# Kernel optimization log

Measured on AMD Instinct MI355X. Metric: run time of the kernel, lower is better.

## Reference

```python
import jax, jax.numpy as jnp
import numpy as np

B, T, D, S, K = 8, 4096, 1024, 64, 3
EPS = 1e-5

def setup_inputs() -> dict:
    key = jax.random.key(0)
    ks = jax.random.split(key, 10)
    def lin(k, out_d, in_d):
        s = 1.0 / np.sqrt(in_d)
        return jax.random.uniform(k, (out_d, in_d), jnp.float32, -s, s)
    return {
        "x": jax.random.normal(ks[0], (B, T, D), jnp.float32),
        "norm_w": jnp.ones((D,), jnp.float32),
        "norm_b": jnp.zeros((D,), jnp.float32),
        "in_w": lin(ks[1], 2 * D, D),
        "in_b": jnp.zeros((2 * D,), jnp.float32),
        "conv_w": jax.random.normal(ks[2], (D, 1, K), jnp.float32) / np.sqrt(K),
        "conv_b": jnp.zeros((D,), jnp.float32),
        "dt_w": lin(ks[3], S, D),
        "dt_b": jnp.zeros((S,), jnp.float32),
        "b_w": lin(ks[4], S, D),
        "b_b": jnp.zeros((S,), jnp.float32),
        "c_w": lin(ks[5], S, D),
        "c_b": jnp.zeros((S,), jnp.float32),
        "a_log": jax.random.normal(ks[6], (S,), jnp.float32) * 0.02,
        "d": jnp.ones((D,), jnp.float32),
        "out_w": lin(ks[7], D, D + S),
        "out_b": jnp.zeros((D,), jnp.float32),
    }

def reference(x, norm_w, norm_b, in_w, in_b, conv_w, conv_b,
              dt_w, dt_b, b_w, b_b, c_w, c_b, a_log, d, out_w, out_b):
    bsz, tlen, dim = x.shape
    sdim = a_log.shape[0]
    k = conv_w.shape[-1]
    residual = x
    # LayerNorm
    mu = jnp.mean(x, axis=-1, keepdims=True)
    var = jnp.mean(jnp.square(x - mu), axis=-1, keepdims=True)
    xn = (x - mu) * jax.lax.rsqrt(var + EPS) * norm_w + norm_b
    # in_proj and chunk
    h = xn @ in_w.T + in_b                       # (B,T,2D)
    x_proj, z = jnp.split(h, 2, axis=-1)         # each (B,T,D)
    # depthwise conv over time, 'same' padding
    xc = jax.lax.conv_general_dilated(
        x_proj.transpose(0, 2, 1), conv_w, (1,), [(k // 2, k // 2)],
        dimension_numbers=("NCH", "OIH", "NCH"), feature_group_count=dim)
    x_conv = jnp.tanh((xc + conv_b[None, :, None]).transpose(0, 2, 1))  # (B,T,D)
    # gate projections for all timesteps at once
    dt = jax.nn.softplus(z @ dt_w.T + dt_b) + 1e-4   # (B,T,S)
    b = jnp.tanh(z @ b_w.T + b_b)                    # (B,T,S)
    c = jnp.tanh(z @ c_w.T + c_b)                    # (B,T,S)
    a = -jnp.exp(a_log)                              # (S,)
    decay = jnp.exp(a * dt)                          # (B,T,S)
    # linear recurrence: state_t = state_{t-1} * decay_t + b_t
    def step(state, inp):
        dec_t, b_t = inp
        state = state * dec_t + b_t
        return state, state
    _, states = jax.lax.scan(step, jnp.zeros((bsz, sdim), x.dtype),
                             (decay.transpose(1, 0, 2), b.transpose(1, 0, 2)))
    states = states.transpose(1, 0, 2)               # (B,T,S)
    y = c * states
    mix = jnp.concatenate([x_conv * d, y], axis=-1)  # (B,T,D+S)
    out = mix @ out_w.T + out_b                      # (B,T,D)
    return residual + out
```

## Files before the change

kernel.cpp:

```cpp
#include <hip/hip_runtime.h>

#define TT 4096
#define DD 1024
#define NN 32768

typedef short s16x8 __attribute__((ext_vector_type(8)));
typedef float f32x4 __attribute__((ext_vector_type(4)));
typedef unsigned short ushort_t;

__device__ __forceinline__ unsigned short f2bf(float f) {
  unsigned u = __float_as_uint(f);
  u += 0x7FFFu + ((u >> 16) & 1u);
  return (unsigned short)(u >> 16);
}
__device__ __forceinline__ float bf2f(unsigned short h) {
  return __uint_as_float(((unsigned)h) << 16);
}
__device__ __forceinline__ void load_lds16(const void* g, void* l) {
  __builtin_amdgcn_global_load_lds(
      (const __attribute__((address_space(1))) unsigned int*)g,
      (__attribute__((address_space(3))) unsigned int*)l, 16, 0, 0);
}

__global__ __launch_bounds__(256)
void cvt_kernel(const float* __restrict__ s, ushort_t* __restrict__ d, int n) {
  int i = (blockIdx.x * 256 + threadIdx.x) * 4;
  if (i < n) {
    float4 v = *(const float4*)&s[i];
    ushort4 o; o.x = f2bf(v.x); o.y = f2bf(v.y); o.z = f2bf(v.z); o.w = f2bf(v.w);
    *(ushort4*)&d[i] = o;
  }
}

__global__ __launch_bounds__(256)
void w3pad_kernel(const float* __restrict__ dt_w, const float* __restrict__ b_w,
                  const float* __restrict__ c_w, ushort_t* __restrict__ w3) {
  int e = (blockIdx.x * 256 + threadIdx.x) * 4;
  int row = e >> 10, col = e & 1023;
  float4 v; v.x = 0.f; v.y = 0.f; v.z = 0.f; v.w = 0.f;
  if (row < 64)       v = *(const float4*)&dt_w[(row << 10) + col];
  else if (row < 128) v = *(const float4*)&b_w[((row - 64) << 10) + col];
  else if (row < 192) v = *(const float4*)&c_w[((row - 128) << 10) + col];
  ushort4 o; o.x = f2bf(v.x); o.y = f2bf(v.y); o.z = f2bf(v.z); o.w = f2bf(v.w);
  *(ushort4*)&w3[e] = o;
}

__global__ __launch_bounds__(256)
void ln_kernel(const float* __restrict__ x, const float* __restrict__ w,
               const float* __restrict__ bv, ushort_t* __restrict__ xn)
{
  int row = blockIdx.x * 4 + (threadIdx.x >> 6);
  int lane = threadIdx.x & 63;
  const float* xr = x + (size_t)row * DD;
  float4 v[4];
  float s = 0.f, ss = 0.f;
  #pragma unroll
  for (int j = 0; j < 4; ++j) {
    v[j] = *(const float4*)&xr[j * 256 + lane * 4];
    s  += v[j].x + v[j].y + v[j].z + v[j].w;
    ss += v[j].x * v[j].x + v[j].y * v[j].y + v[j].z * v[j].z + v[j].w * v[j].w;
  }
  #pragma unroll
  for (int off = 32; off > 0; off >>= 1) {
    s  += __shfl_xor(s, off, 64);
    ss += __shfl_xor(ss, off, 64);
  }
  float mean = s * (1.f / 1024.f);
  float var  = ss * (1.f / 1024.f) - mean * mean;
  float rinv = rsqrtf(var + 1e-5f);
  #pragma unroll
  for (int j = 0; j < 4; ++j) {
    int c = j * 256 + lane * 4;
    float4 wv = *(const float4*)&w[c];
    float4 bb = *(const float4*)&bv[c];
    ushort4 o;
    o.x = f2bf((v[j].x - mean) * rinv * wv.x + bb.x);
    o.y = f2bf((v[j].y - mean) * rinv * wv.y + bb.y);
    o.z = f2bf((v[j].z - mean) * rinv * wv.z + bb.z);
    o.w = f2bf((v[j].w - mean) * rinv * wv.w + bb.w);
    *(ushort4*)&xn[(size_t)row * DD + c] = o;
  }
}

template<int EP>
__global__ __launch_bounds__(512, 2)
void gemm256(const ushort_t* __restrict__ A, const ushort_t* __restrict__ W,
             int M, int N, int K,
             const float* __restrict__ bias0, const float* __restrict__ bias1,
             const float* __restrict__ bias2, const float* __restrict__ alog,
             ushort_t* __restrict__ o0, ushort_t* __restrict__ o1,
             float* __restrict__ g0, float* __restrict__ g1, float* __restrict__ g2,
             const float* __restrict__ resid, float* __restrict__ outf)
{
  __shared__ ushort_t lds[65536];
  const int tid = threadIdx.x;
  const int lane = tid & 63;
  const int wid = tid >> 6;
  const int wr = wid >> 2;
  const int wc = wid & 3;
  const int lane15 = lane & 15;
  const int lgrp = lane >> 4;
  const int rsw = (lane15 & 7) << 4;
  const int ntn = N >> 8;
  int bid = blockIdx.x;
  { const int cpx = (int)gridDim.x >> 3; bid = (bid & 7) * cpx + (bid >> 3); }
  const int brow = (bid / ntn) << 8;
  const int bcol = (bid % ntn) << 8;
  const int nk = K >> 6;
  const int sRow = tid >> 3;
  const int sCol = (tid & 7) << 4;
  const char* ldsb = (const char*)lds;
  (void)M;

#define STG(bufb, isB, h, kt) do { \
    const int ktc_ = (kt) < nk ? (kt) : nk - 1; \
    const ushort_t* gsrc_ = (isB) ? W : A; \
    const int rowb_ = ((isB) ? bcol : brow) + (h) * 128; \
    _Pragma("unroll") \
    for (int j_ = 0; j_ < 2; ++j_) { \
      const int r_ = j_ * 64 + sRow; \
      load_lds16((const char*)(gsrc_ + (size_t)(rowb_ + r_) * K) + ktc_ * 128 + (sCol ^ ((r_ & 7) << 4)), \
                 (char*)lds + (bufb) * 65536 + (isB) * 32768 + (h) * 16384 + r_ * 128 + sCol); \
    } } while (0)

#define LDA_(bufb, m, kk) \
  (*(const s16x8*)(ldsb + (bufb) * 65536 + wr * 16384 + ((m) * 16 + lane15) * 128 + (((kk) * 64 + lgrp * 16) ^ rsw)))
#define LDB_(bufb, n, kk) \
  (*(const s16x8*)(ldsb + (bufb) * 65536 + 32768 + (wc >> 1) * 16384 + ((wc & 1) * 64 + (n) * 16 + lane15) * 128 + (((kk) * 64 + lgrp * 16) ^ rsw)))

#define BARR() asm volatile("s_barrier" ::: "memory")
#define VMW4() asm volatile("s_waitcnt vmcnt(4)" ::: "memory")
#define SBAR() __builtin_amdgcn_sched_barrier(0)

#define RD_A(bufb, mh) do { \
    _Pragma("unroll") for (int kk = 0; kk < 2; ++kk) \
    _Pragma("unroll") for (int q = 0; q < 4; ++q) \
      af[kk][q] = LDA_(bufb, (mh) * 4 + q, kk); } while (0)
#define RD_B(bufb, nh) do { \
    _Pragma("unroll") for (int kk = 0; kk < 2; ++kk) \
    _Pragma("unroll") for (int p = 0; p < 2; ++p) \
      bfr[nh][kk][p] = LDB_(bufb, (nh) * 2 + p, kk); } while (0)

#define MFMAQ(mh, nh) do { \
    __builtin_amdgcn_s_setprio(1); \
    _Pragma("unroll") for (int kk = 0; kk < 2; ++kk) \
    _Pragma("unroll") for (int q = 0; q < 4; ++q) \
    _Pragma("unroll") for (int p = 0; p < 2; ++p) \
      acc[(mh) * 4 + q][(nh) * 2 + p] = __builtin_amdgcn_mfma_f32_16x16x32_bf16( \
          af[kk][q], bfr[nh][kk][p], acc[(mh) * 4 + q][(nh) * 2 + p], 0, 0, 0); \
    __builtin_amdgcn_s_setprio(0); } while (0)

  f32x4 acc[8][4];
  #pragma unroll
  for (int m = 0; m < 8; ++m) {
    #pragma unroll
    for (int n = 0; n < 4; ++n) acc[m][n] = (f32x4){0.f, 0.f, 0.f, 0.f};
  }
  s16x8 af[2][4];
  s16x8 bfr[2][2][2];

  STG(0, 1, 0, 0); STG(0, 0, 0, 0); STG(0, 0, 1, 0); STG(0, 1, 1, 0);
  STG(1, 1, 0, 1); STG(1, 0, 0, 1);
  VMW4(); BARR();
  RD_A(0, 0); RD_B(0, 0);

  const int nIter = nk >> 1;
  for (int it = 0; it < nIter; ++it) {
    const int t0 = 2 * it;
    STG(1, 0, 1, t0 + 1);
    MFMAQ(0, 0); SBAR(); RD_B(0, 1); BARR();
    STG(1, 1, 1, t0 + 1);
    MFMAQ(0, 1); SBAR(); RD_A(0, 1); BARR();
    STG(0, 1, 0, t0 + 2);
    MFMAQ(1, 1); BARR();
    STG(0, 0, 0, t0 + 2);
    VMW4(); BARR();
    MFMAQ(1, 0); SBAR(); RD_A(1, 0); RD_B(1, 0); BARR();
    STG(0, 0, 1, t0 + 2);
    MFMAQ(0, 0); SBAR(); RD_B(1, 1); BARR();
    STG(0, 1, 1, t0 + 2);
    MFMAQ(0, 1); SBAR(); RD_A(1, 1); BARR();
    STG(1, 1, 0, t0 + 3);
    MFMAQ(1, 1); BARR();
    STG(1, 0, 0, t0 + 3);
    VMW4(); BARR();
    MFMAQ(1, 0); SBAR(); RD_A(0, 0); RD_B(0, 0); BARR();
  }
  if (nk & 1) {
    MFMAQ(0, 0); SBAR(); RD_B(0, 1);
    MFMAQ(0, 1); SBAR(); RD_A(0, 1);
    MFMAQ(1, 1);
    MFMAQ(1, 0);
  }

#undef STG
#undef LDA_
#undef LDB_
#undef BARR
#undef VMW4
#undef SBAR
#undef RD_A
#undef RD_B
#undef MFMAQ

  #pragma unroll
  for (int m = 0; m < 8; ++m) {
    #pragma unroll
    for (int i = 0; i < 4; ++i) {
      const int r = brow + wr * 128 + m * 16 + lgrp * 4 + i;
      #pragma unroll
      for (int n = 0; n < 4; ++n) {
        const int col = bcol + wc * 64 + n * 16 + lane15;
        float v = acc[m][n][i];
        if constexpr (EP == 0) {
          v += bias0[col];
          if (col < DD) o0[(size_t)r * DD + col] = f2bf(v);
          else          o1[(size_t)r * DD + (col - DD)] = f2bf(v);
        } else if constexpr (EP == 1) {
          if (col < 64) {
            float u = v + bias0[col];
            float sp = (u > 20.f) ? u : log1pf(expf(u));
            float dt = sp + 1e-4f;
            float a = -expf(alog[col]);
            g0[(size_t)r * 64 + col] = expf(a * dt);
          } else if (col < 128) {
            g1[(size_t)r * 64 + (col - 64)] = tanhf(v + bias1[col - 64]);
          } else if (col < 192) {
            g2[(size_t)r * 64 + (col - 128)] = tanhf(v + bias2[col - 128]);
          }
        } else {
          outf[(size_t)r * DD + col] = v + bias0[col] + resid[(size_t)r * DD + col];
        }
      }
    }
  }
}

template<int EP>
__global__ __launch_bounds__(256)
void gemm128(const ushort_t* __restrict__ A, const ushort_t* __restrict__ W,
             int M, int N, int K,
             const float* __restrict__ bias0, const float* __restrict__ bias1,
             const float* __restrict__ bias2, const float* __restrict__ alog,
             float* __restrict__ g0, float* __restrict__ g1, float* __restrict__ g2)
{
  __shared__ ushort_t As[128 * 64];
  __shared__ ushort_t Bs[128 * 64];
  const int tid = threadIdx.x;
  const int lane = tid & 63;
  const int wid = tid >> 6;
  const int ntn = N >> 7;
  const int brow = (blockIdx.x / ntn) << 7;
  const int bcol = (blockIdx.x % ntn) << 7;
  const int wr = (wid >> 1) << 6;
  const int wc = (wid & 1) << 6;
  const int lane15 = lane & 15;
  const int lgrp = lane >> 4;

  f32x4 acc[4][4];
  #pragma unroll
  for (int m = 0; m < 4; ++m)
    #pragma unroll
    for (int n = 0; n < 4; ++n)
      acc[m][n] = (f32x4){0.f, 0.f, 0.f, 0.f};

  const int r0 = tid >> 3;
  const int c0 = (tid & 7) << 3;
  const ushort_t* gA = A + (size_t)(brow + r0) * K + c0;
  const ushort_t* gW = W + (size_t)(bcol + r0) * K + c0;
  ushort_t* lA = &As[r0 * 64 + c0];
  ushort_t* lB = &Bs[r0 * 64 + c0];

  for (int k0 = 0; k0 < K; k0 += 64) {
    #pragma unroll
    for (int j = 0; j < 4; ++j) {
      load_lds16(gA + (size_t)(j * 32) * K + k0, lA + j * 32 * 64);
      load_lds16(gW + (size_t)(j * 32) * K + k0, lB + j * 32 * 64);
    }
    __syncthreads();
    #pragma unroll
    for (int kk = 0; kk < 2; ++kk) {
      s16x8 af[4], bfr[4];
      #pragma unroll
      for (int m = 0; m < 4; ++m)
        af[m] = *(const s16x8*)&As[(wr + m * 16 + lane15) * 64 + kk * 32 + lgrp * 8];
      #pragma unroll
      for (int n = 0; n < 4; ++n)
        bfr[n] = *(const s16x8*)&Bs[(wc + n * 16 + lane15) * 64 + kk * 32 + lgrp * 8];
      #pragma unroll
      for (int m = 0; m < 4; ++m)
        #pragma unroll
        for (int n = 0; n < 4; ++n)
          acc[m][n] = __builtin_amdgcn_mfma_f32_16x16x32_bf16(af[m], bfr[n], acc[m][n], 0, 0, 0);
    }
    __syncthreads();
  }

  #pragma unroll
  for (int m = 0; m < 4; ++m) {
    #pragma unroll
    for (int i = 0; i < 4; ++i) {
      const int r = brow + wr + m * 16 + lgrp * 4 + i;
      #pragma unroll
      for (int n = 0; n < 4; ++n) {
        const int col = bcol + wc + n * 16 + lane15;
        float v = acc[m][n][i];
        if constexpr (EP == 1) {
          if (col < 64) {
            float u = v + bias0[col];
            float sp = (u > 20.f) ? u : log1pf(expf(u));
            float dt = sp + 1e-4f;
            float a = -expf(alog[col]);
            g0[(size_t)r * 64 + col] = expf(a * dt);
          } else if (col < 128) {
            g1[(size_t)r * 64 + (col - 64)] = tanhf(v + bias1[col - 64]);
          } else if (col < 192) {
            g2[(size_t)r * 64 + (col - 128)] = tanhf(v + bias2[col - 128]);
          }
        }
      }
    }
  }
}

__global__ __launch_bounds__(256)
void conv_kernel(const ushort_t* __restrict__ xp, const float* __restrict__ cw,
                 const float* __restrict__ cb, const float* __restrict__ dvec,
                 ushort_t* __restrict__ mix)
{
  int idx = blockIdx.x * 256 + threadIdx.x;
  int row = idx >> 7;
  int d0 = (idx & 127) << 3;
  int t = row & (TT - 1);
  s16x8 cur = *(const s16x8*)&xp[(size_t)row * DD + d0];
  s16x8 prv; s16x8 nxt;
  #pragma unroll
  for (int j = 0; j < 8; ++j) { prv[j] = 0; nxt[j] = 0; }
  if (t > 0)      prv = *(const s16x8*)&xp[(size_t)(row - 1) * DD + d0];
  if (t < TT - 1) nxt = *(const s16x8*)&xp[(size_t)(row + 1) * DD + d0];
  float wv[24];
  #pragma unroll
  for (int j = 0; j < 6; ++j) *(float4*)&wv[j * 4] = *(const float4*)&cw[d0 * 3 + j * 4];
  float cbv[8], dv[8];
  *(float4*)&cbv[0] = *(const float4*)&cb[d0];
  *(float4*)&cbv[4] = *(const float4*)&cb[d0 + 4];
  *(float4*)&dv[0]  = *(const float4*)&dvec[d0];
  *(float4*)&dv[4]  = *(const float4*)&dvec[d0 + 4];
  s16x8 o;
  #pragma unroll
  for (int j = 0; j < 8; ++j) {
    float acc = cbv[j] + bf2f((ushort_t)prv[j]) * wv[j * 3]
              + bf2f((ushort_t)cur[j]) * wv[j * 3 + 1]
              + bf2f((ushort_t)nxt[j]) * wv[j * 3 + 2];
    o[j] = (short)f2bf(tanhf(acc) * dv[j]);
  }
  *(s16x8*)&mix[(size_t)row * 1088 + d0] = o;
}

__global__ void scanA_kernel(const float* __restrict__ dec, const float* __restrict__ bb,
                             float* __restrict__ P, float* __restrict__ Q)
{
  int b = blockIdx.x >> 6, ci = blockIdx.x & 63, s = threadIdx.x;
  size_t base = (((size_t)b * TT) + ci * 64) * 64 + s;
  float p = 1.f, q = 0.f;
  #pragma unroll 4
  for (int t = 0; t < 64; ++t) {
    float d = dec[base + (size_t)t * 64];
    float w = bb[base + (size_t)t * 64];
    q = q * d + w; p *= d;
  }
  int o = (b * 64 + ci) * 64 + s;
  P[o] = p; Q[o] = q;
}

__global__ void scanB_kernel(const float* __restrict__ P, const float* __restrict__ Q,
                             float* __restrict__ I)
{
  int b = blockIdx.x, s = threadIdx.x;
  float st = 0.f;
  for (int ci = 0; ci < 64; ++ci) {
    int o = (b * 64 + ci) * 64 + s;
    I[o] = st;
    st = st * P[o] + Q[o];
  }
}

__global__ void scanC_kernel(const float* __restrict__ dec, const float* __restrict__ bb,
                             const float* __restrict__ cc, const float* __restrict__ I,
                             ushort_t* __restrict__ mix)
{
  int b = blockIdx.x >> 6, ci = blockIdx.x & 63, s = threadIdx.x;
  size_t base = (((size_t)b * TT) + ci * 64) * 64 + s;
  float st = I[(b * 64 + ci) * 64 + s];
  size_t mrow = (size_t)b * TT + ci * 64;
  #pragma unroll 4
  for (int t = 0; t < 64; ++t) {
    size_t o = base + (size_t)t * 64;
    st = st * dec[o] + bb[o];
    mix[(mrow + t) * 1088 + 1024 + s] = (ushort_t)f2bf(cc[o] * st);
  }
}

extern "C" void kernel_launch(void* const* d_in, const int* in_sizes, int n_in,
                              void* d_out, int out_size, void* d_ws, size_t ws_size,
                              hipStream_t stream)
{
  (void)in_sizes; (void)n_in; (void)out_size; (void)ws_size;
  const float* x      = (const float*)d_in[0];
  const float* norm_w = (const float*)d_in[1];
  const float* norm_b = (const float*)d_in[2];
  const float* in_w   = (const float*)d_in[3];
  const float* in_b   = (const float*)d_in[4];
  const float* conv_w = (const float*)d_in[5];
  const float* conv_b = (const float*)d_in[6];
  const float* dt_w   = (const float*)d_in[7];
  const float* dt_b   = (const float*)d_in[8];
  const float* b_w    = (const float*)d_in[9];
  const float* b_b    = (const float*)d_in[10];
  const float* c_w    = (const float*)d_in[11];
  const float* c_b    = (const float*)d_in[12];
  const float* a_log  = (const float*)d_in[13];
  const float* dvec   = (const float*)d_in[14];
  const float* out_w  = (const float*)d_in[15];
  const float* out_b  = (const float*)d_in[16];
  float* out = (float*)d_out;

  char* p = (char*)d_ws;
  ushort_t* mix    = (ushort_t*)p;
  ushort_t* xn     = mix;
  p += 71303168;
  ushort_t* xproj  = (ushort_t*)p; p += 67108864;
  ushort_t* z      = (ushort_t*)p; p += 67108864;
  ushort_t* inw_bf = (ushort_t*)p; p += 4194304;
  ushort_t* w3     = (ushort_t*)p; p += 524288;
  ushort_t* outw_bf= (ushort_t*)p; p += 2228224;
  float* P = (float*)p; p += 131072;
  float* Q = (float*)p; p += 131072;
  float* I = (float*)p; p += 131072;
  float* gdec = (float*)xproj;
  float* gbb  = (float*)((char*)xproj + 8388608);
  float* gcc  = (float*)((char*)xproj + 16777216);

  cvt_kernel<<<2048, 256, 0, stream>>>(in_w,  inw_bf,  2097152);
  cvt_kernel<<<1088, 256, 0, stream>>>(out_w, outw_bf, 1114112);
  w3pad_kernel<<<256, 256, 0, stream>>>(dt_w, b_w, c_w, w3);
  ln_kernel<<<8192, 256, 0, stream>>>(x, norm_w, norm_b, xn);

  gemm256<0><<<(NN / 256) * (2048 / 256), 512, 0, stream>>>(
      xn, inw_bf, NN, 2048, 1024,
      in_b, nullptr, nullptr, nullptr,
      xproj, z, nullptr, nullptr, nullptr, nullptr, nullptr);

  conv_kernel<<<NN * 128 / 256, 256, 0, stream>>>(xproj, conv_w, conv_b, dvec, mix);

  gemm128<1><<<(NN / 128) * (256 / 128), 256, 0, stream>>>(
      z, w3, NN, 256, 1024,
      dt_b, b_b, c_b, a_log,
      gdec, gbb, gcc);

  scanA_kernel<<<512, 64, 0, stream>>>(gdec, gbb, P, Q);
  scanB_kernel<<<8, 64, 0, stream>>>(P, Q, I);
  scanC_kernel<<<512, 64, 0, stream>>>(gdec, gbb, gcc, I, mix);

  gemm256<2><<<(NN / 256) * (1024 / 256), 512, 0, stream>>>(
      mix, outw_bf, NN, 1024, 1088,
      out_b, nullptr, nullptr, nullptr,
      nullptr, nullptr, nullptr, nullptr, nullptr, x, out);
}
```

Measured before the change: 426.4 us.

## Double-buffer MFMA fragment registers and drop sched barriers in GEMM main loop

Splits the A and B register fragments into ping-pong sets (afP/afQ, b0/b1) so LDS reads for the next quadrant can be issued while MFMAs on the current quadrant run, and removes the sched_barrier fences between compute and reads. It also reorders the quadrant traversal (snake order) and moves the vmcnt wait earlier with a smaller count. The aim is to hide LDS read latency behind matrix ops. The cost is higher VGPR pressure, and the changed waitcnt placement could affect correctness or occupancy.

Result: no change. 423.4 us (-0.7%).

```diff
diff --git a/kernel.cpp b/kernel.cpp
--- a/kernel.cpp
+++ b/kernel.cpp
@@ -129,25 +129,25 @@
   (*(const s16x8*)(ldsb + (bufb) * 65536 + 32768 + (wc >> 1) * 16384 + ((wc & 1) * 64 + (n) * 16 + lane15) * 128 + (((kk) * 64 + lgrp * 16) ^ rsw)))
 
 #define BARR() asm volatile("s_barrier" ::: "memory")
+#define VMW2() asm volatile("s_waitcnt vmcnt(2)" ::: "memory")
 #define VMW4() asm volatile("s_waitcnt vmcnt(4)" ::: "memory")
-#define SBAR() __builtin_amdgcn_sched_barrier(0)
-
-#define RD_A(bufb, mh) do { \
+
+#define RDA(dst, bufb, mh) do { \
     _Pragma("unroll") for (int kk = 0; kk < 2; ++kk) \
     _Pragma("unroll") for (int q = 0; q < 4; ++q) \
-      af[kk][q] = LDA_(bufb, (mh) * 4 + q, kk); } while (0)
-#define RD_B(bufb, nh) do { \
+      dst[kk][q] = LDA_(bufb, (mh) * 4 + q, kk); } while (0)
+#define RDB(dst, bufb, nh) do { \
     _Pragma("unroll") for (int kk = 0; kk < 2; ++kk) \
     _Pragma("unroll") for (int p = 0; p < 2; ++p) \
-      bfr[nh][kk][p] = LDB_(bufb, (nh) * 2 + p, kk); } while (0)
-
-#define MFMAQ(mh, nh) do { \
+      dst[kk][p] = LDB_(bufb, (nh) * 2 + p, kk); } while (0)
+
+#define MFMAQ(AF, BF, mh, nh) do { \
     __builtin_amdgcn_s_setprio(1); \
     _Pragma("unroll") for (int kk = 0; kk < 2; ++kk) \
     _Pragma("unroll") for (int q = 0; q < 4; ++q) \
     _Pragma("unroll") for (int p = 0; p < 2; ++p) \
       acc[(mh) * 4 + q][(nh) * 2 + p] = __builtin_amdgcn_mfma_f32_16x16x32_bf16( \
-          af[kk][q], bfr[nh][kk][p], acc[(mh) * 4 + q][(nh) * 2 + p], 0, 0, 0); \
+          AF[kk][q], BF[kk][p], acc[(mh) * 4 + q][(nh) * 2 + p], 0, 0, 0); \
     __builtin_amdgcn_s_setprio(0); } while (0)
 
   f32x4 acc[8][4];
@@ -156,51 +156,59 @@
     #pragma unroll
     for (int n = 0; n < 4; ++n) acc[m][n] = (f32x4){0.f, 0.f, 0.f, 0.f};
   }
-  s16x8 af[2][4];
-  s16x8 bfr[2][2][2];
+  s16x8 afP[2][4], afQ[2][4];
+  s16x8 b0[2][2], b1[2][2];
 
   STG(0, 1, 0, 0); STG(0, 0, 0, 0); STG(0, 0, 1, 0); STG(0, 1, 1, 0);
   STG(1, 1, 0, 1); STG(1, 0, 0, 1);
   VMW4(); BARR();
-  RD_A(0, 0); RD_B(0, 0);
+  RDA(afP, 0, 0); RDB(b0, 0, 0);
 
   const int nIter = nk >> 1;
   for (int it = 0; it < nIter; ++it) {
     const int t0 = 2 * it;
     STG(1, 0, 1, t0 + 1);
-    MFMAQ(0, 0); SBAR(); RD_B(0, 1); BARR();
+    MFMAQ(afP, b0, 0, 0);
+    RDB(b1, 0, 1); BARR();
     STG(1, 1, 1, t0 + 1);
-    MFMAQ(0, 1); SBAR(); RD_A(0, 1); BARR();
+    MFMAQ(afP, b1, 0, 1);
+    RDA(afQ, 0, 1); BARR();
     STG(0, 1, 0, t0 + 2);
-    MFMAQ(1, 1); BARR();
+    MFMAQ(afQ, b1, 1, 1);
+    VMW2(); BARR();
     STG(0, 0, 0, t0 + 2);
-    VMW4(); BARR();
-    MFMAQ(1, 0); SBAR(); RD_A(1, 0); RD_B(1, 0); BARR();
+    MFMAQ(afQ, b0, 1, 0);
+    RDA(afP, 1, 0); RDB(b1, 1, 1); BARR();
     STG(0, 0, 1, t0 + 2);
-    MFMAQ(0, 0); SBAR(); RD_B(1, 1); BARR();
+    MFMAQ(afP, b1, 0, 1);
+    RDB(b0, 1, 0); BARR();
     STG(0, 1, 1, t0 + 2);
-    MFMAQ(0, 1); SBAR(); RD_A(1, 1); BARR();
+    MFMAQ(afP, b0, 0, 0);
+    RDA(afQ, 1, 1); BARR();
     STG(1, 1, 0, t0 + 3);
-    MFMAQ(1, 1); BARR();
+    MFMAQ(afQ, b0, 1, 0);
+    VMW2(); BARR();
     STG(1, 0, 0, t0 + 3);
-    VMW4(); BARR();
-    MFMAQ(1, 0); SBAR(); RD_A(0, 0); RD_B(0, 0); BARR();
+    MFMAQ(afQ, b1, 1, 1);
+    RDA(afP, 0, 0); RDB(b0, 0, 0); BARR();
   }
   if (nk & 1) {
-    MFMAQ(0, 0); SBAR(); RD_B(0, 1);
-    MFMAQ(0, 1); SBAR(); RD_A(0, 1);
-    MFMAQ(1, 1);
-    MFMAQ(1, 0);
+    MFMAQ(afP, b0, 0, 0);
+    RDB(b1, 0, 1);
+    MFMAQ(afP, b1, 0, 1);
+    RDA(afQ, 0, 1);
+    MFMAQ(afQ, b1, 1, 1);
+    MFMAQ(afQ, b0, 1, 0);
   }
 
 #undef STG
 #undef LDA_
 #undef LDB_
 #undef BARR
+#undef VMW2
 #undef VMW4
-#undef SBAR
-#undef RD_A
-#undef RD_B
+#undef RDA
+#undef RDB
 #undef MFMAQ
 
   #pragma unroll
```
